# Kernel tuning notes

Measured on AMD Instinct MI355X. Metric: run time of the kernel, lower is better.

The kernel has to match this reference:

```python
import jax, jax.numpy as jnp
import numpy as np

N_NODES = 50000

def setup_inputs() -> dict:
    key = jax.random.key(0)
    ks = jax.random.split(key, 7)
    N, E, D, O = N_NODES, 800000, 64, 64
    x = jax.random.normal(ks[0], (N, D), dtype=jnp.float32)
    src = jax.random.randint(ks[1], (E,), 0, N, dtype=jnp.int32)
    dst = jax.random.randint(ks[2], (E,), 0, N, dtype=jnp.int32)
    s = 1.0 / np.sqrt(D)
    W_self = jax.random.uniform(ks[3], (D, O), jnp.float32, -s, s)
    b_self = jax.random.uniform(ks[4], (O,), jnp.float32, -s, s)
    W_neigh = jax.random.uniform(ks[5], (D, O), jnp.float32, -s, s)
    b_neigh = jax.random.uniform(ks[6], (O,), jnp.float32, -s, s)
    return {"x": x, "src": src, "dst": dst, "W_self": W_self, "b_self": b_self,
            "W_neigh": W_neigh, "b_neigh": b_neigh}

def reference(x, src, dst, W_self, b_self, W_neigh, b_neigh):
    # SAGEConv mean aggregator: h_neigh[v] = mean_{(u->v) in E} x[u]
    msgs = x[src]                                        # [E, D] gather
    agg = jax.ops.segment_sum(msgs, dst, num_segments=x.shape[0])   # [N, D]
    deg = jax.ops.segment_sum(jnp.ones_like(dst, dtype=x.dtype), dst,
                              num_segments=x.shape[0])   # [N]
    h_neigh = agg / jnp.maximum(deg, 1.0)[:, None]
    # rst = fc_self(h_dst) + fc_neigh(h_neigh)
    return (x @ W_self + b_self) + (h_neigh @ W_neigh + b_neigh)
```

## Files before the change

### kernel.cpp

```cpp
#include <hip/hip_runtime.h>


typedef _Float16 half2_t __attribute__((ext_vector_type(2)));

__device__ __forceinline__ unsigned pack_bf2(float a, float b) {
    unsigned ua = __builtin_bit_cast(unsigned, a);
    unsigned ub = __builtin_bit_cast(unsigned, b);
    ua += 0x7fffu + ((ua >> 16) & 1u);
    ub += 0x7fffu + ((ub >> 16) & 1u);
    return (ua >> 16) | (ub & 0xffff0000u);
}

__global__ __launch_bounds__(256) void zero_int(int* __restrict__ p, int n) {
    int i = blockIdx.x * 256 + threadIdx.x;
    if (i < n) p[i] = 0;
}

__global__ __launch_bounds__(256) void build_transform(
    const float* __restrict__ x,
    const int* __restrict__ src,
    const int* __restrict__ dst,
    const float* __restrict__ Wself,
    const float* __restrict__ bself,
    const float* __restrict__ Wneigh,
    const float* __restrict__ bneigh,
    int* __restrict__ cnt,
    unsigned short* __restrict__ csr16,
    _Float16* __restrict__ y16,
    float* __restrict__ out,
    int N, int E)
{
    __shared__ unsigned sW[64 * 64];
    __shared__ float    sx[16 * 64];

    int t   = threadIdx.x;
    int gid = blockIdx.x * 256 + t;

    if (gid < E) {
        int d = dst[gid];
        int pos = atomicAdd(&cnt[d], 1);
        if (pos < 64)
            csr16[(d << 6) + pos] = (unsigned short)src[gid];
    }

    for (int i = t; i < 64 * 64; i += 256)
        sW[i] = pack_bf2(Wself[i], Wneigh[i]);

    int lane = t & 63;
    int w    = t >> 6;
    int vbase = blockIdx.x * 16 + w * 4;

    for (int n = 0; n < 4; ++n) {
        int v = vbase + n;
        if (v < N) sx[(w * 4 + n) * 64 + lane] = x[(size_t)v * 64 + lane];
    }
    __syncthreads();

    float bias = bself[lane] + bneigh[lane];
    float aS0 = bias, aS1 = bias, aS2 = bias, aS3 = bias;
    float aN0 = 0.f,  aN1 = 0.f,  aN2 = 0.f,  aN3 = 0.f;

#pragma unroll 16
    for (int d = 0; d < 64; ++d) {
        unsigned wv = sW[d * 64 + lane];
        float ws = __builtin_bit_cast(float, wv << 16);
        float wn = __builtin_bit_cast(float, wv & 0xffff0000u);
        float x0 = sx[(w * 4 + 0) * 64 + d];
        float x1 = sx[(w * 4 + 1) * 64 + d];
        float x2 = sx[(w * 4 + 2) * 64 + d];
        float x3 = sx[(w * 4 + 3) * 64 + d];
        aS0 += x0 * ws; aN0 += x0 * wn;
        aS1 += x1 * ws; aN1 += x1 * wn;
        aS2 += x2 * ws; aN2 += x2 * wn;
        aS3 += x3 * ws; aN3 += x3 * wn;
    }

    float accS[4] = {aS0, aS1, aS2, aS3};
    float accN[4] = {aN0, aN1, aN2, aN3};
    for (int n = 0; n < 4; ++n) {
        int v = vbase + n;
        if (v < N) {
            out[(size_t)v * 64 + lane] = accS[n];
            y16[(size_t)v * 64 + lane] = (_Float16)accN[n];
        }
    }
}

__global__ __launch_bounds__(256) void gather_mean(
    const unsigned* __restrict__ y16w,
    const unsigned short* __restrict__ csr16,
    const int* __restrict__ cnt,
    float* __restrict__ out,
    int N)
{
    int t    = threadIdx.x;
    int lane = t & 63;
    int w    = t >> 6;
    int l5   = lane & 31;
    int half = lane >> 5;

    int vbase = blockIdx.x * 16 + w * 4;

    for (int n = 0; n < 4; ++n) {
        int v = vbase + n;
        if (v >= N) break;
        int dg = cnt[v];
        int m  = min(dg, 64);
        int cs = (int)csr16[(v << 6) + lane];

        half2_t pk0 = {(_Float16)0, (_Float16)0};
        half2_t pk1 = {(_Float16)0, (_Float16)0};

        int j = 0;
        for (; j + 3 < m; j += 4) {
            int s0 = __builtin_amdgcn_readlane(cs, j);
            int s1 = __builtin_amdgcn_readlane(cs, j + 1);
            int s2 = __builtin_amdgcn_readlane(cs, j + 2);
            int s3 = __builtin_amdgcn_readlane(cs, j + 3);
            int uA = half ? s1 : s0;
            int uB = half ? s3 : s2;
            unsigned vA = y16w[(uA << 5) + l5];
            unsigned vB = y16w[(uB << 5) + l5];
            pk0 += __builtin_bit_cast(half2_t, vA);
            pk1 += __builtin_bit_cast(half2_t, vB);
        }
        for (; j + 1 < m; j += 2) {
            int s0 = __builtin_amdgcn_readlane(cs, j);
            int s1 = __builtin_amdgcn_readlane(cs, j + 1);
            int uA = half ? s1 : s0;
            unsigned vA = y16w[(uA << 5) + l5];
            pk0 += __builtin_bit_cast(half2_t, vA);
        }
        if (j < m) {
            int s0 = __builtin_amdgcn_readlane(cs, j);
            if (half == 0) {
                unsigned vA = y16w[(s0 << 5) + l5];
                pk0 += __builtin_bit_cast(half2_t, vA);
            }
        }

        half2_t pk = pk0 + pk1;
        unsigned mine  = __builtin_bit_cast(unsigned, pk);
        unsigned other = (unsigned)__shfl_xor((int)mine, 32, 64);
        half2_t tot = pk + __builtin_bit_cast(half2_t, other);

        float inv = 1.0f / fmaxf((float)dg, 1.0f);
        float m0 = (float)tot.x * inv;
        float m1 = (float)tot.y * inv;

        if (half == 0) {
            float2* po = (float2*)(out + (size_t)v * 64) + l5;
            float2 p = *po;
            p.x += m0; p.y += m1;
            *po = p;
        }
    }
}

extern "C" void kernel_launch(void* const* d_in, const int* in_sizes, int n_in,
                              void* d_out, int out_size, void* d_ws, size_t ws_size,
                              hipStream_t stream) {
    const float* x      = (const float*)d_in[0];
    const int*   src    = (const int*)d_in[1];
    const int*   dst    = (const int*)d_in[2];
    const float* Wself  = (const float*)d_in[3];
    const float* bself  = (const float*)d_in[4];
    const float* Wneigh = (const float*)d_in[5];
    const float* bneigh = (const float*)d_in[6];
    float* out = (float*)d_out;

    int N = in_sizes[0] / 64;
    int E = in_sizes[1];

    int*            cnt   = (int*)d_ws;
    unsigned short* csr16 = (unsigned short*)(cnt + N);
    _Float16*       y16   = (_Float16*)(csr16 + (size_t)N * 64);

    zero_int<<<(N + 255) / 256, 256, 0, stream>>>(cnt, N);

    int nb = (max(E, N * 16) + 255) / 256;
    build_transform<<<nb, 256, 0, stream>>>(
        x, src, dst, Wself, bself, Wneigh, bneigh,
        cnt, csr16, y16, out, N, E);

    gather_mean<<<(N + 15) / 16, 256, 0, stream>>>(
        (const unsigned*)y16, csr16, cnt, out, N);
}
```

Measured before the change: 155.1 us.

## Use 16-byte gathers with 8 neighbors per wave; broadcast x via readlane

The neighbor gather now has each group of 8 lanes load one full 128-byte fp16 row as uint4. Eight neighbors are processed per wave iteration and combined with an xor-shuffle tree, replacing 4-byte loads over two half-waves. Nodes with zero degree are skipped early. In the transform kernel, x rows stay in registers and are broadcast with readlane instead of being staged through shared memory, and the d loop is fully unrolled. The gather change aims to cut load instruction count and raise bytes per request, at the cost of more shuffles and a masked tail iteration.

```diff
diff --git a/kernel.cpp b/kernel.cpp
--- a/kernel.cpp
+++ b/kernel.cpp
@@ -31,7 +31,6 @@
     int N, int E)
 {
     __shared__ unsigned sW[64 * 64];
-    __shared__ float    sx[16 * 64];
 
     int t   = threadIdx.x;
     int gid = blockIdx.x * 256 + t;
@@ -50,25 +49,32 @@
     int w    = t >> 6;
     int vbase = blockIdx.x * 16 + w * 4;
 
-    for (int n = 0; n < 4; ++n) {
-        int v = vbase + n;
-        if (v < N) sx[(w * 4 + n) * 64 + lane] = x[(size_t)v * 64 + lane];
-    }
+    float xv0 = 0.f, xv1 = 0.f, xv2 = 0.f, xv3 = 0.f;
+    if (vbase + 0 < N) xv0 = x[(size_t)(vbase + 0) * 64 + lane];
+    if (vbase + 1 < N) xv1 = x[(size_t)(vbase + 1) * 64 + lane];
+    if (vbase + 2 < N) xv2 = x[(size_t)(vbase + 2) * 64 + lane];
+    if (vbase + 3 < N) xv3 = x[(size_t)(vbase + 3) * 64 + lane];
+
     __syncthreads();
 
     float bias = bself[lane] + bneigh[lane];
     float aS0 = bias, aS1 = bias, aS2 = bias, aS3 = bias;
     float aN0 = 0.f,  aN1 = 0.f,  aN2 = 0.f,  aN3 = 0.f;
 
-#pragma unroll 16
+    int ix0 = __builtin_bit_cast(int, xv0);
+    int ix1 = __builtin_bit_cast(int, xv1);
+    int ix2 = __builtin_bit_cast(int, xv2);
+    int ix3 = __builtin_bit_cast(int, xv3);
+
+#pragma unroll
     for (int d = 0; d < 64; ++d) {
         unsigned wv = sW[d * 64 + lane];
         float ws = __builtin_bit_cast(float, wv << 16);
         float wn = __builtin_bit_cast(float, wv & 0xffff0000u);
-        float x0 = sx[(w * 4 + 0) * 64 + d];
-        float x1 = sx[(w * 4 + 1) * 64 + d];
-        float x2 = sx[(w * 4 + 2) * 64 + d];
-        float x3 = sx[(w * 4 + 3) * 64 + d];
+        float x0 = __builtin_bit_cast(float, __builtin_amdgcn_readlane(ix0, d));
+        float x1 = __builtin_bit_cast(float, __builtin_amdgcn_readlane(ix1, d));
+        float x2 = __builtin_bit_cast(float, __builtin_amdgcn_readlane(ix2, d));
+        float x3 = __builtin_bit_cast(float, __builtin_amdgcn_readlane(ix3, d));
         aS0 += x0 * ws; aN0 += x0 * wn;
         aS1 += x1 * ws; aN1 += x1 * wn;
         aS2 += x2 * ws; aN2 += x2 * wn;
@@ -87,7 +93,7 @@
 }
 
 __global__ __launch_bounds__(256) void gather_mean(
-    const unsigned* __restrict__ y16w,
+    const uint4* __restrict__ y16v,
     const unsigned short* __restrict__ csr16,
     const int* __restrict__ cnt,
     float* __restrict__ out,
@@ -96,8 +102,8 @@
     int t    = threadIdx.x;
     int lane = t & 63;
     int w    = t >> 6;
-    int l5   = lane & 31;
-    int half = lane >> 5;
+    int q    = lane >> 3;
+    int l3   = lane & 7;
 
     int vbase = blockIdx.x * 16 + w * 4;
 
@@ -105,54 +111,54 @@
         int v = vbase + n;
         if (v >= N) break;
         int dg = cnt[v];
-        int m  = min(dg, 64);
+        if (dg <= 0) continue;
+        int m = min(dg, 64);
         int cs = (int)csr16[(v << 6) + lane];
 
-        half2_t pk0 = {(_Float16)0, (_Float16)0};
-        half2_t pk1 = {(_Float16)0, (_Float16)0};
+        int a0 = 0, a1 = 0, a2 = 0, a3 = 0;
 
-        int j = 0;
-        for (; j + 3 < m; j += 4) {
-            int s0 = __builtin_amdgcn_readlane(cs, j);
-            int s1 = __builtin_amdgcn_readlane(cs, j + 1);
-            int s2 = __builtin_amdgcn_readlane(cs, j + 2);
-            int s3 = __builtin_amdgcn_readlane(cs, j + 3);
-            int uA = half ? s1 : s0;
-            int uB = half ? s3 : s2;
-            unsigned vA = y16w[(uA << 5) + l5];
-            unsigned vB = y16w[(uB << 5) + l5];
-            pk0 += __builtin_bit_cast(half2_t, vA);
-            pk1 += __builtin_bit_cast(half2_t, vB);
-        }
-        for (; j + 1 < m; j += 2) {
-            int s0 = __builtin_amdgcn_readlane(cs, j);
-            int s1 = __builtin_amdgcn_readlane(cs, j + 1);
-            int uA = half ? s1 : s0;
-            unsigned vA = y16w[(uA << 5) + l5];
-            pk0 += __builtin_bit_cast(half2_t, vA);
-        }
-        if (j < m) {
-            int s0 = __builtin_amdgcn_readlane(cs, j);
-            if (half == 0) {
-                unsigned vA = y16w[(s0 << 5) + l5];
-                pk0 += __builtin_bit_cast(half2_t, vA);
+        for (int j = 0; j < m; j += 8) {
+            int jq  = j + q;
+            int jc  = jq < m - 1 ? jq : m - 1;
+            int u   = __shfl(cs, jc, 64);
+            uint4 L = y16v[((size_t)u << 3) + l3];
+            if (jq < m) {
+                half2_t p0 = __builtin_bit_cast(half2_t, a0) + __builtin_bit_cast(half2_t, L.x);
+                half2_t p1 = __builtin_bit_cast(half2_t, a1) + __builtin_bit_cast(half2_t, L.y);
+                half2_t p2 = __builtin_bit_cast(half2_t, a2) + __builtin_bit_cast(half2_t, L.z);
+                half2_t p3 = __builtin_bit_cast(half2_t, a3) + __builtin_bit_cast(half2_t, L.w);
+                a0 = __builtin_bit_cast(int, p0);
+                a1 = __builtin_bit_cast(int, p1);
+                a2 = __builtin_bit_cast(int, p2);
+                a3 = __builtin_bit_cast(int, p3);
             }
         }
 
-        half2_t pk = pk0 + pk1;
-        unsigned mine  = __builtin_bit_cast(unsigned, pk);
-        unsigned other = (unsigned)__shfl_xor((int)mine, 32, 64);
-        half2_t tot = pk + __builtin_bit_cast(half2_t, other);
+#pragma unroll
+        for (int s = 8; s <= 32; s <<= 1) {
+            half2_t p0 = __builtin_bit_cast(half2_t, a0) + __builtin_bit_cast(half2_t, __shfl_xor(a0, s, 64));
+            half2_t p1 = __builtin_bit_cast(half2_t, a1) + __builtin_bit_cast(half2_t, __shfl_xor(a1, s, 64));
+            half2_t p2 = __builtin_bit_cast(half2_t, a2) + __builtin_bit_cast(half2_t, __shfl_xor(a2, s, 64));
+            half2_t p3 = __builtin_bit_cast(half2_t, a3) + __builtin_bit_cast(half2_t, __shfl_xor(a3, s, 64));
+            a0 = __builtin_bit_cast(int, p0);
+            a1 = __builtin_bit_cast(int, p1);
+            a2 = __builtin_bit_cast(int, p2);
+            a3 = __builtin_bit_cast(int, p3);
+        }
 
-        float inv = 1.0f / fmaxf((float)dg, 1.0f);
-        float m0 = (float)tot.x * inv;
-        float m1 = (float)tot.y * inv;
-
-        if (half == 0) {
-            float2* po = (float2*)(out + (size_t)v * 64) + l5;
-            float2 p = *po;
-            p.x += m0; p.y += m1;
-            *po = p;
+        if (q == 0) {
+            float inv = 1.0f / (float)dg;
+            half2_t h0 = __builtin_bit_cast(half2_t, a0);
+            half2_t h1 = __builtin_bit_cast(half2_t, a1);
+            half2_t h2 = __builtin_bit_cast(half2_t, a2);
+            half2_t h3 = __builtin_bit_cast(half2_t, a3);
+            float4* po = (float4*)(out + (size_t)v * 64) + l3 * 2;
+            float4 p0 = po[0], p1 = po[1];
+            p0.x += (float)h0.x * inv; p0.y += (float)h0.y * inv;
+            p0.z += (float)h1.x * inv; p0.w += (float)h1.y * inv;
+            p1.x += (float)h2.x * inv; p1.y += (float)h2.y * inv;
+            p1.z += (float)h3.x * inv; p1.w += (float)h3.y * inv;
+            po[0] = p0; po[1] = p1;
         }
     }
 }
@@ -184,5 +190,5 @@
         cnt, csr16, y16, out, N, E);
 
     gather_mean<<<(N + 15) / 16, 256, 0, stream>>>(
-        (const unsigned*)y16, csr16, cnt, out, N);
+        (const uint4*)y16, csr16, cnt, out, N);
 }
```

Result: no change. 153.4 us (-1.1%).
